# Performance work log

Measured on AMD Instinct MI355X. Metric: run time of the kernel, lower is better.

Reference implementation:

```python
import jax, jax.numpy as jnp
import numpy as np

N_U = 100000; N_I = 100000; D = 64; Q = 5
N_E = 2000000; L = 2; B = 4096; P = 10
TEMP = 0.2; LAM1 = 0.2; LAM2 = 0.2
DROPOUT = 0.1; EPS = 0.1


def setup_inputs() -> dict:
    key = jax.random.key(0)
    ks = jax.random.split(key, 20)
    s = 0.05  # xavier-ish init scale
    return {
        'E_u_0': jax.random.normal(ks[0], (N_U, D), jnp.float32) * s,
        'E_i_0': jax.random.normal(ks[1], (N_I, D), jnp.float32) * s,
        'adj_vals': jax.random.uniform(ks[2], (N_E,), jnp.float32) * 0.05,
        'u_mul_s': jax.random.normal(ks[3], (N_U, Q), jnp.float32) * s,
        'v_mul_s': jax.random.normal(ks[4], (N_I, Q), jnp.float32) * s,
        'ut': jax.random.normal(ks[5], (Q, N_U), jnp.float32) * s,
        'vt': jax.random.normal(ks[6], (Q, N_I), jnp.float32) * s,
        'W_nn': jax.random.normal(ks[7], (D, D), jnp.float32) * s,
        'W_dd': jax.random.normal(ks[8], (D, D), jnp.float32) * s,
        'W_ng': jax.random.normal(ks[9], (L, D, D), jnp.float32) * s,
        'W_dg': jax.random.normal(ks[10], (L, D, D), jnp.float32) * s,
        'W_nd': jax.random.normal(ks[11], (L, D, D), jnp.float32) * s,
        'adj_rows': jax.random.randint(ks[12], (N_E,), 0, N_U),
        'adj_cols': jax.random.randint(ks[13], (N_E,), 0, N_I),
        'uids': jax.random.randint(ks[14], (B,), 0, N_U),
        'iids': jax.random.randint(ks[15], (B,), 0, N_I),
        'pos': jax.random.randint(ks[16], (B, P), 0, N_I),
        'neg': jax.random.randint(ks[17], (B, P), 0, N_I),
    }


def _act(x):  # LeakyReLU(0.5)
    return jnp.where(x >= 0, x, 0.5 * x)


def _l2n(x):  # F.normalize(p=2, dim=1)
    return x / jnp.maximum(jnp.linalg.norm(x, axis=1, keepdims=True), 1e-12)


def _spmm(vals, rows, cols, X, n_out):
    # out[r] = sum_e vals[e] * X[cols[e]]
    return jax.ops.segment_sum(vals[:, None] * X[cols], rows, num_segments=n_out)


def _info_nce(gnn_raw, hyper_raw, W, mask):
    gnn = _l2n(gnn_raw)
    hyper = _l2n(hyper_raw) @ W
    pos_score = jnp.exp(jnp.sum(gnn * hyper, axis=1) / TEMP)
    neg_score = jnp.exp(gnn @ hyper.T / TEMP).sum(axis=1)
    return (-jnp.log(pos_score / (neg_score + 1e-8) + 1e-8) * mask).sum()


def _mk_mask(k):
    return (jax.random.uniform(k, (B,)) > 0.5).astype(jnp.float32)


def _forward(E_u_0, E_i_0, adj_vals, u_mul_s, v_mul_s, ut, vt, W_nn, W_dd, W_ng, W_dg, W_nd,
             adj_rows, adj_cols, uids, iids, pos, neg):
    rkey = jax.random.key(42)
    keep = 1.0 - DROPOUT
    E_u_list = [E_u_0]; E_i_list = [E_i_0]
    Z_u_list = [None]; Z_i_list = [None]
    Z_du_list = [None]; Z_di_list = [None]
    G_u_list = [None]; G_i_list = [None]
    for _ in range(L):
        rkey, k1, k2, k3, k4 = jax.random.split(rkey, 5)
        Eu_p, Ei_p = E_u_list[-1], E_i_list[-1]
        # sparse dropout (independent masks, as in torch code) + spmm + LeakyReLU
        v1 = adj_vals * jax.random.bernoulli(k1, keep, adj_vals.shape) / keep
        Z_du = _act(_spmm(v1, adj_rows, adj_cols, Ei_p, N_U))
        v2 = adj_vals * jax.random.bernoulli(k2, keep, adj_vals.shape) / keep
        Z_di = _act(_spmm(v2, adj_cols, adj_rows, Eu_p, N_I))
        # noise-augmented view
        Z_u = _act(_spmm(adj_vals, adj_rows, adj_cols, Ei_p, N_U))
        Z_u = Z_u + jnp.sign(Z_u) * _l2n(jax.random.uniform(k3, Eu_p.shape)) * EPS
        Z_i = _act(_spmm(adj_vals, adj_cols, adj_rows, Eu_p, N_I))
        Z_i = Z_i + jnp.sign(Z_i) * _l2n(jax.random.uniform(k4, Ei_p.shape)) * EPS
        # SVD (global) view
        G_u = _act(u_mul_s @ (vt @ Ei_p))
        G_i = _act(v_mul_s @ (ut @ Eu_p))
        Z_u_list.append(Z_u); Z_i_list.append(Z_i)
        Z_du_list.append(Z_du); Z_di_list.append(Z_di)
        G_u_list.append(G_u); G_i_list.append(G_i)
        E_u_list.append(Z_u + Z_du + Eu_p)
        E_i_list.append(Z_i + Z_di + Ei_p)
    E_u = E_u_list[0]
    for t in E_u_list[1:]:
        E_u = E_u + t
    E_i = E_i_list[0]
    for t in E_i_list[1:]:
        E_i = E_i + t

    mkey = jax.random.key(7)
    def L_loss(ids, Zl, Gl, Wstack, key):
        out = jnp.float32(0.0)
        for l in range(1, L + 1):
            key, km = jax.random.split(key)
            out = out + _info_nce(Zl[l][ids], Gl[l][ids], Wstack[l - 1], _mk_mask(km))
        return out, key
    def inter_loss(ids, Zl, W, key):
        key, km = jax.random.split(key)
        return _info_nce(Zl[1][ids], Zl[2][ids], W, _mk_mask(km)), key

    loss_n_u, mkey = L_loss(uids, Z_u_list, G_u_list, W_ng, mkey)
    loss_n_i, mkey = L_loss(iids, Z_i_list, G_i_list, W_ng, mkey)
    loss_nn_u, mkey = inter_loss(uids, Z_u_list, W_nn, mkey)
    loss_nn_i, mkey = inter_loss(iids, Z_i_list, W_nn, mkey)
    loss_d_u, mkey = L_loss(uids, Z_du_list, G_u_list, W_dg, mkey)
    loss_d_i, mkey = L_loss(iids, Z_di_list, G_i_list, W_dg, mkey)
    loss_dd_u, mkey = inter_loss(uids, Z_du_list, W_dd, mkey)
    loss_dd_i, mkey = inter_loss(iids, Z_di_list, W_dd, mkey)
    loss_nd_u, mkey = L_loss(uids, Z_u_list, Z_du_list, W_nd, mkey)
    loss_nd_i, mkey = L_loss(iids, Z_i_list, Z_di_list, W_nd, mkey)
    loss_n = loss_n_u + loss_n_i
    loss_d = loss_d_u + loss_d_i
    loss_nn = loss_nn_u + loss_nn_i
    loss_dd = loss_dd_u + loss_dd_i
    loss_nd = loss_nd_u + loss_nd_i

    # U_IConstLoss, vectorized over the batch
    u_emb = E_u[uids]                       # [B, D]
    pos_emb = E_i[pos]                      # [B, P, D]
    neg_emb = E_i[neg]                      # [B, P, D]
    pos_sc = jnp.einsum('bd,bpd->bp', u_emb, pos_emb)
    neg_sc = jnp.einsum('bd,bpd->bp', u_emb, neg_emb)
    pos_d = pos_sc.min(axis=1)
    neg_d = neg_sc.max(axis=1)
    hard = jnp.where(neg_d - pos_d > 0.005, 10.0 * (neg_d - pos_d), 0.0)
    bpr = jnp.maximum(1.0 - pos_sc + neg_sc, 0.0).sum(axis=1)
    loss_r = (bpr + hard).sum() / B

    loss = loss_r + LAM1 * (loss_n + loss_d) + LAM2 * (loss_nn + loss_dd + loss_nd)
    return (loss, loss_r, loss_d, loss_n)


def reference(E_u_0, E_i_0, adj_vals, u_mul_s, v_mul_s, ut, vt, W_nn, W_dd, W_ng, W_dg, W_nd,
              adj_rows, adj_cols, uids, iids, pos, neg):
    return _forward(E_u_0, E_i_0, adj_vals, u_mul_s, v_mul_s, ut, vt, W_nn, W_dd, W_ng, W_dg, W_nd,
                    adj_rows, adj_cols, uids, iids, pos, neg)
```

## Files before the change

kernel.cpp:

```cpp
#include <hip/hip_runtime.h>
#include <hip/hip_bf16.h>
#include <cstdint>

#define C_NU 100000
#define C_NI 100000
#define C_DIM 64
#define C_Q 5
#define C_NE 2000000
#define C_B 4096
#define C_P 10
#define NROW 100000
#define NCB 196
#define NCHK 256
#define CHUNK 7813

typedef unsigned short u16;
typedef unsigned char u8;
typedef __attribute__((ext_vector_type(8))) short short8;
typedef __attribute__((ext_vector_type(4))) float f32x4;

__device__ static inline int rfl(int v) { return __builtin_amdgcn_readfirstlane(v); }
__device__ static inline uint32_t rflu(uint32_t v) {
  return (uint32_t)__builtin_amdgcn_readfirstlane((int)v);
}

__host__ __device__ static inline void tf2x32(uint32_t k0, uint32_t k1,
                                              uint32_t& x0, uint32_t& x1) {
  uint32_t k2 = k0 ^ k1 ^ 0x1BD11BDAu;
#define TFR(r) { x0 += x1; x1 = (x1 << r) | (x1 >> (32 - r)); x1 ^= x0; }
  x0 += k0; x1 += k1;
  TFR(13) TFR(15) TFR(26) TFR(6)
  x0 += k1; x1 += k2 + 1u;
  TFR(17) TFR(29) TFR(16) TFR(24)
  x0 += k2; x1 += k0 + 2u;
  TFR(13) TFR(15) TFR(26) TFR(6)
  x0 += k0; x1 += k1 + 3u;
  TFR(17) TFR(29) TFR(16) TFR(24)
  x0 += k1; x1 += k2 + 4u;
  TFR(13) TFR(15) TFR(26) TFR(6)
  x0 += k2; x1 += k0 + 5u;
#undef TFR
}

__device__ static inline float tf_uniform(uint32_t k0, uint32_t k1, uint32_t idx) {
  uint32_t x0 = 0u, x1 = idx;
  tf2x32(k0, k1, x0, x1);
  uint32_t bits = x0 ^ x1;
  return __uint_as_float((bits >> 9) | 0x3F800000u) - 1.0f;
}

__device__ static inline float leaky(float x) { return x >= 0.f ? x : 0.5f * x; }

__device__ static inline u16 f2bf(float f) {
  uint32_t x = __float_as_uint(f);
  return (u16)((x + 0x7FFFu + ((x >> 16) & 1u)) >> 16);
}
__device__ static inline float bf2f(u16 u) {
  return __uint_as_float((uint32_t)u << 16);
}

__device__ static inline u8 f2fp8(float x) {
  float t = x * 256.f;
  uint32_t sgn = (__float_as_uint(t) >> 24) & 0x80u;
  float a = fabsf(t) * 0x1p-120f;
  uint32_t u = __float_as_uint(a);
  u += 0x7FFFFu + ((u >> 20) & 1u);
  uint32_t mag = u >> 20;
  if (mag > 0x7Fu) mag = 0x7Fu;
  return (u8)(sgn | mag);
}

__constant__ int c_gsel[16] = {0,1,2,3, 0,2, 4,5,6,7, 4,6, 0,1,2,3};
__constant__ int c_hsrc[16] = {8,9,10,11, 1,3, 8,9,10,11, 5,7, 4,5,6,7};
__constant__ int c_wsel[16] = {0,1,0,1, 2,2, 3,4,3,4, 5,5, 6,7,6,7};
__constant__ int c_slot[16] = {0,0,0,0, 2,2, 1,1,1,1, 3,3, 4,4,4,4};

struct WPtrs { const float* W[8]; };
struct NceKeys { uint32_t k0[16]; uint32_t k1[16]; };
struct DropKeys { uint32_t a[8]; };


__global__ __launch_bounds__(256) void passA_hist(
    const int* __restrict__ rows, const int* __restrict__ cols,
    uint32_t* __restrict__ cntA) {
  __shared__ uint32_t h[NCB];
  const int dir = blockIdx.y, c = blockIdx.x, t = threadIdx.x;
  for (int i = t; i < NCB; i += 256) h[i] = 0u;
  __syncthreads();
  const int e0 = c * CHUNK, e1 = min(e0 + CHUNK, C_NE);
  const int* ids = dir ? cols : rows;
  for (int e = e0 + t; e < e1; e += 256) atomicAdd(&h[ids[e] >> 9], 1u);
  __syncthreads();
  for (int i = t; i < NCB; i += 256) cntA[(dir * NCB + i) * NCHK + c] = h[i];
}

__global__ __launch_bounds__(512) void scanA1(
    const uint32_t* __restrict__ cntA, uint32_t* __restrict__ offs,
    uint32_t* __restrict__ bsum) {
  __shared__ uint32_t s[512];
  const int b = blockIdx.x, t = threadIdx.x;
  const int idx = b * 512 + t;
  uint32_t v = cntA[idx];
  s[t] = v;
  __syncthreads();
  for (int off = 1; off < 512; off <<= 1) {
    uint32_t a = (t >= off) ? s[t - off] : 0u;
    __syncthreads();
    s[t] += a;
    __syncthreads();
  }
  offs[idx] = s[t] - v;
  if (t == 511) bsum[b] = s[511];
}

__global__ __launch_bounds__(256) void scanA2(
    const uint32_t* __restrict__ bsum, uint32_t* __restrict__ boff) {
  __shared__ uint32_t s[256];
  const int t = threadIdx.x;
  uint32_t v = (t < NCB) ? bsum[t] : 0u;
  s[t] = v;
  __syncthreads();
  for (int off = 1; off < 256; off <<= 1) {
    uint32_t a = (t >= off) ? s[t - off] : 0u;
    __syncthreads();
    s[t] += a;
    __syncthreads();
  }
  if (t < NCB) boff[t] = s[t] - v;
}

__global__ __launch_bounds__(512) void scanA3(
    uint32_t* __restrict__ offs, const uint32_t* __restrict__ boff) {
  offs[blockIdx.x * 512 + threadIdx.x] += boff[blockIdx.x];
}

__global__ __launch_bounds__(256) void passA_scatter(
    const int* __restrict__ rows, const int* __restrict__ cols,
    const float* __restrict__ vals, const uint32_t* __restrict__ offs,
    uint2* __restrict__ edgesA, DropKeys dk) {
  __shared__ uint32_t lofs[NCB];
  const int dir = blockIdx.y, c = blockIdx.x, t = threadIdx.x;
  for (int i = t; i < NCB; i += 256) lofs[i] = offs[(dir * NCB + i) * NCHK + c];
  __syncthreads();
  const int e0 = c * CHUNK, e1 = min(e0 + CHUNK, C_NE);
  const uint32_t kA0 = dk.a[dir * 4 + 0], kA1 = dk.a[dir * 4 + 1];
  const uint32_t kB0 = dk.a[dir * 4 + 2], kB1 = dk.a[dir * 4 + 3];
  for (int e = e0 + t; e < e1; e += 256) {
    const int r = rows[e], cc = cols[e];
    const int dst = dir ? cc : r, src = dir ? r : cc;
    const uint32_t kl0 = (tf_uniform(kA0, kA1, (uint32_t)e) < 0.9f) ? 1u : 0u;
    const uint32_t kl1 = (tf_uniform(kB0, kB1, (uint32_t)e) < 0.9f) ? 1u : 0u;
    const uint32_t x = (uint32_t)src | (kl0 << 17) | (kl1 << 18) |
                       ((uint32_t)(dst & 511) << 19);
    const uint32_t pos = atomicAdd(&lofs[dst >> 9], 1u);
    edgesA[pos] = make_uint2(x, __float_as_uint(vals[e]));
  }
}

__global__ __launch_bounds__(512) void passB_kernel(
    const uint2* __restrict__ edgesA, const uint32_t* __restrict__ offs,
    uint2* __restrict__ edgesB, uint32_t* __restrict__ starts) {
  __shared__ uint32_t cnt[512];
  __shared__ uint32_t scn[512];
  const int dir = blockIdx.y, cb = blockIdx.x, t = threadIdx.x;
  const uint32_t segStart = offs[(dir * NCB + cb) * NCHK];
  const uint32_t segEnd = (dir == 1 && cb == NCB - 1)
                              ? (uint32_t)(2 * C_NE)
                              : offs[(dir * NCB + cb + 1) * NCHK];
  cnt[t] = 0u;
  __syncthreads();
  for (uint32_t e = segStart + t; e < segEnd; e += 512)
    atomicAdd(&cnt[(edgesA[e].x >> 19) & 511u], 1u);
  __syncthreads();
  uint32_t v = cnt[t];
  scn[t] = v;
  __syncthreads();
  for (int off = 1; off < 512; off <<= 1) {
    uint32_t a = (t >= off) ? scn[t - off] : 0u;
    __syncthreads();
    scn[t] += a;
    __syncthreads();
  }
  const uint32_t rstart = segStart + scn[t] - v;
  const int grow = cb * 512 + t;
  if (grow < NROW) starts[dir * (NROW + 1) + grow] = rstart;
  if (cb == NCB - 1 && t == 0) starts[dir * (NROW + 1) + NROW] = segEnd;
  cnt[t] = rstart;
  __syncthreads();
  for (uint32_t e = segStart + t; e < segEnd; e += 512) {
    const uint2 q = edgesA[e];
    const uint32_t pos = atomicAdd(&cnt[(q.x >> 19) & 511u], 1u);
    edgesB[pos] = q;
  }
}

__global__ __launch_bounds__(256) void fp8_convert(
    const float* __restrict__ src, u8* __restrict__ dst, int n4) {
  int i = blockIdx.x * 256 + threadIdx.x;
  if (i >= n4) return;
  float4 v = ((const float4*)src)[i];
  uint32_t o = (uint32_t)f2fp8(v.x) | ((uint32_t)f2fp8(v.y) << 8) |
               ((uint32_t)f2fp8(v.z) << 16) | ((uint32_t)f2fp8(v.w) << 24);
  ((uint32_t*)dst)[i] = o;
}

__global__ __launch_bounds__(256) void w16_prep(WPtrs wp, u16* __restrict__ Wt16) {
  int i = blockIdx.x * 256 + threadIdx.x;
  if (i >= 8 * 4096) return;
  int w = i >> 12, kd = i & 4095, k = kd >> 6, d = kd & 63;
  Wt16[w * 4096 + d * 64 + k] = f2bf(wp.W[w][k * 64 + d]);
}

__global__ __launch_bounds__(256) void spmm_row(
    const uint2* __restrict__ edges, const uint32_t* __restrict__ starts,
    const u8* __restrict__ Einf, const float* __restrict__ Eprev,
    float* __restrict__ Enext, u8* __restrict__ Enf8,
    u16* __restrict__ Zout, u16* __restrict__ Zdout,
    uint32_t nk0, uint32_t nk1, int layer) {
  const int row = rfl(blockIdx.x * 4 + (threadIdx.x >> 6));
  const int lane = threadIdx.x & 63;
  if (row >= NROW) return;
  const uint32_t s0 = rflu(starts[row]);
  const uint32_t s1 = rflu(starts[row + 1]);
  const uint32_t kbit = 1u << (17 + layer);
  const float VS = 0x1p112f;
  float z = 0.f, zd = 0.f;
  uint32_t e = s0;
  for (; e + 4 <= s1; e += 4) {
    const uint32_t p0 = rflu(edges[e].x),     w0 = rflu(edges[e].y);
    const uint32_t p1 = rflu(edges[e + 1].x), w1 = rflu(edges[e + 1].y);
    const uint32_t p2 = rflu(edges[e + 2].x), w2 = rflu(edges[e + 2].y);
    const uint32_t p3 = rflu(edges[e + 3].x), w3 = rflu(edges[e + 3].y);
    const uint32_t b0 = Einf[(size_t)(p0 & 0x1FFFFu) * 64 + lane];
    const uint32_t b1 = Einf[(size_t)(p1 & 0x1FFFFu) * 64 + lane];
    const uint32_t b2 = Einf[(size_t)(p2 & 0x1FFFFu) * 64 + lane];
    const uint32_t b3 = Einf[(size_t)(p3 & 0x1FFFFu) * 64 + lane];
    const float x0 = __uint_as_float(((b0 & 0x80u) << 24) | ((b0 & 0x7Fu) << 20));
    const float x1 = __uint_as_float(((b1 & 0x80u) << 24) | ((b1 & 0x7Fu) << 20));
    const float x2 = __uint_as_float(((b2 & 0x80u) << 24) | ((b2 & 0x7Fu) << 20));
    const float x3 = __uint_as_float(((b3 & 0x80u) << 24) | ((b3 & 0x7Fu) << 20));
    const float v0 = __uint_as_float(w0) * VS, v1 = __uint_as_float(w1) * VS;
    const float v2 = __uint_as_float(w2) * VS, v3 = __uint_as_float(w3) * VS;
    const float d0 = (p0 & kbit) ? v0 : 0.f;
    const float d1 = (p1 & kbit) ? v1 : 0.f;
    const float d2 = (p2 & kbit) ? v2 : 0.f;
    const float d3 = (p3 & kbit) ? v3 : 0.f;
    z += v0 * x0; zd += d0 * x0;
    z += v1 * x1; zd += d1 * x1;
    z += v2 * x2; zd += d2 * x2;
    z += v3 * x3; zd += d3 * x3;
  }
  for (; e < s1; ++e) {
    const uint32_t p = rflu(edges[e].x), wv = rflu(edges[e].y);
    const uint32_t b = Einf[(size_t)(p & 0x1FFFFu) * 64 + lane];
    const float x = __uint_as_float(((b & 0x80u) << 24) | ((b & 0x7Fu) << 20));
    const float v = __uint_as_float(wv) * VS;
    z += v * x;
    zd += ((p & kbit) ? v : 0.f) * x;
  }
  z = leaky(z);
  zd = leaky(zd * (1.0f / 0.9f));
  const float u = tf_uniform(nk0, nk1, (uint32_t)row * 64u + (uint32_t)lane);
  float ss = u * u;
#pragma unroll
  for (int off = 1; off < 64; off <<= 1) ss += __shfl_xor(ss, off);
  const float nrm = fmaxf(sqrtf(ss), 1e-12f);
  const float sg = (z > 0.f) ? 1.f : (z < 0.f ? -1.f : 0.f);
  z += sg * (u / nrm) * 0.1f;
  const size_t j = (size_t)row * 64 + lane;
  Zout[j] = f2bf(z);
  Zdout[j] = f2bf(zd);
  if (Enext) {
    const float en = z + zd + Eprev[j];
    Enext[j] = en;
    Enf8[j] = f2fp8(en);
  }
}

__global__ __launch_bounds__(256) void svd_reduce2(
    const float* __restrict__ T0, const float* __restrict__ E0,
    const float* __restrict__ T1, const float* __restrict__ E1,
    float* __restrict__ Mu, float* __restrict__ Mi) {
  const int dir = blockIdx.y;
  const float* __restrict__ T = dir ? T1 : T0;
  const float* __restrict__ E = dir ? E1 : E0;
  float* __restrict__ M = dir ? Mi : Mu;
  const int lane = threadIdx.x & 63;
  const int wl = threadIdx.x >> 6;
  const int gw = blockIdx.x * 4 + wl;
  float a0 = 0.f, a1 = 0.f, a2 = 0.f, a3 = 0.f, a4 = 0.f;
  for (int i = gw; i < NROW; i += 4096) {
    const float x = E[(size_t)i * 64 + lane];
    a0 += T[i] * x;
    a1 += T[NROW + i] * x;
    a2 += T[2 * NROW + i] * x;
    a3 += T[3 * NROW + i] * x;
    a4 += T[4 * NROW + i] * x;
  }
  __shared__ float red[4][5][64];
  red[wl][0][lane] = a0; red[wl][1][lane] = a1; red[wl][2][lane] = a2;
  red[wl][3][lane] = a3; red[wl][4][lane] = a4;
  __syncthreads();
  for (int o = threadIdx.x; o < 320; o += 256) {
    const int q = o >> 6, d = o & 63;
    const float s = red[0][q][d] + red[1][q][d] + red[2][q][d] + red[3][q][d];
    atomicAdd(&M[o], s);
  }
}

__global__ __launch_bounds__(256) void gather_norm(
    const int* __restrict__ ids, const u16* __restrict__ Z,
    const u16* __restrict__ Zd, const float* __restrict__ mul_s,
    const float* __restrict__ M, u16* __restrict__ oZ,
    u16* __restrict__ oZd, u16* __restrict__ oG) {
  long long t = (long long)blockIdx.x * blockDim.x + threadIdx.x;
  int b = (int)(t >> 6);
  int d = (int)(t & 63);
  if (b >= C_B) return;
  int id = rfl(ids[b]);
  float v;
  u16* out;
  if (blockIdx.y == 0) { v = bf2f(Z[(size_t)id * 64 + d]); out = oZ; }
  else if (blockIdx.y == 1) { v = bf2f(Zd[(size_t)id * 64 + d]); out = oZd; }
  else {
    float s = 0.f;
#pragma unroll
    for (int q = 0; q < 5; ++q) s += mul_s[(size_t)id * 5 + q] * M[q * 64 + d];
    v = leaky(s);
    out = oG;
  }
  float ss = v * v;
#pragma unroll
  for (int off = 1; off < 64; off <<= 1) ss += __shfl_xor(ss, off);
  float nrm = fmaxf(sqrtf(ss), 1e-12f);
  out[(size_t)b * 64 + d] = f2bf(v / nrm);
}

__global__ __launch_bounds__(256) void hyper_mfma(
    const u16* __restrict__ nb, const u16* __restrict__ Wt16,
    u16* __restrict__ hy) {
  const int call = blockIdx.y;
  const int b0 = blockIdx.x * 64;
  __shared__ u16 Xs[64 * 64];
  __shared__ u16 Ws[64 * 64];
  const int tid = threadIdx.x, lane = tid & 63, wid = tid >> 6;
  const u16* X = nb + (size_t)c_hsrc[call] * C_B * 64;
  const u16* Wt = Wt16 + (size_t)c_wsel[call] * 4096;
  {
    const int r = tid >> 2, seg = tid & 3;
    const int base = r * 128 + seg * 32, sw = (r & 7) << 4;
    const uint4* sx = (const uint4*)&X[(size_t)(b0 + r) * 64 + seg * 16];
    uint4 a = sx[0], b = sx[1];
    *(uint4*)((char*)Xs + (base ^ sw)) = a;
    *(uint4*)((char*)Xs + ((base + 16) ^ sw)) = b;
    const uint4* sv = (const uint4*)&Wt[r * 64 + seg * 16];
    uint4 c = sv[0], d = sv[1];
    *(uint4*)((char*)Ws + (base ^ sw)) = c;
    *(uint4*)((char*)Ws + ((base + 16) ^ sw)) = d;
  }
  __syncthreads();
  const int am = (wid << 4) + (lane & 15);
  short8 af[2];
#pragma unroll
  for (int ks = 0; ks < 2; ++ks) {
    const int off = (am * 128 + ks * 64 + ((lane >> 4) << 4)) ^ ((am & 7) << 4);
    af[ks] = *(const short8*)((const char*)Xs + off);
  }
  const int ob = b0 + (wid << 4) + ((lane >> 4) << 2);
#pragma unroll
  for (int n = 0; n < 4; ++n) {
    const int bn = (n << 4) + (lane & 15);
    f32x4 acc = {0.f, 0.f, 0.f, 0.f};
#pragma unroll
    for (int ks = 0; ks < 2; ++ks) {
      const int off = (bn * 128 + ks * 64 + ((lane >> 4) << 4)) ^ ((bn & 7) << 4);
      short8 bf = *(const short8*)((const char*)Ws + off);
      acc = __builtin_amdgcn_mfma_f32_16x16x32_bf16(af[ks], bf, acc, 0, 0, 0);
    }
    const int d = (n << 4) + (lane & 15);
#pragma unroll
    for (int j = 0; j < 4; ++j)
      hy[(size_t)call * C_B * 64 + (size_t)(ob + j) * 64 + d] =
          f2bf(acc[j] * 7.2134752f);
  }
}

__global__ __launch_bounds__(256) void nce_partial(
    const u16* __restrict__ nb, const u16* __restrict__ hy,
    float* __restrict__ rsbuf, float* __restrict__ psbuf) {
  const int call = blockIdx.z;
  const int jc = blockIdx.y;
  const u16* G = nb + (size_t)c_gsel[call] * C_B * 64;
  const u16* H = hy + (size_t)call * C_B * 64;
  const int br = blockIdx.x * 128;
  const int jt0 = jc * 16;
  __shared__ u16 Gs[128 * 64];
  __shared__ u16 Hs[2][64 * 64];
  const int tid = threadIdx.x, lane = tid & 63, wid = tid >> 6;
  {
    const int r2 = tid >> 1;
    const int sw2 = (r2 & 7) << 4;
#pragma unroll
    for (int p = 0; p < 2; ++p) {
      const int sg = (tid & 1) + p * 2;
      const uint4* src = (const uint4*)&G[(size_t)(br + r2) * 64 + sg * 16];
      uint4 a = src[0], b = src[1];
      const int bse = r2 * 128 + sg * 32;
      *(uint4*)((char*)Gs + (bse ^ sw2)) = a;
      *(uint4*)((char*)Gs + ((bse + 16) ^ sw2)) = b;
    }
  }
  const int r = tid >> 2, seg = tid & 3;
  const int base = r * 128 + seg * 32, sw = (r & 7) << 4;
  {
    const uint4* src = (const uint4*)&H[(size_t)(jt0 * 64 + r) * 64 + seg * 16];
    uint4 a = src[0], b = src[1];
    *(uint4*)((char*)Hs[0] + (base ^ sw)) = a;
    *(uint4*)((char*)Hs[0] + ((base + 16) ^ sw)) = b;
  }
  float rs[2] = {0.f, 0.f}, ps[2] = {0.f, 0.f};
  short8 bfG[2][2];
  const int jt_diag = (blockIdx.x << 1) + (wid >> 1);
  const int hsd0 = (wid & 1) << 1;
  int cur = 0;
  for (int jt = jt0; jt < jt0 + 16; ++jt) {
    __syncthreads();
    if (jt == jt0) {
#pragma unroll
      for (int s = 0; s < 2; ++s)
#pragma unroll
        for (int ks = 0; ks < 2; ++ks) {
          const int gc = (wid << 5) + (s << 4) + (lane & 15);
          const int off = (gc * 128 + ks * 64 + ((lane >> 4) << 4)) ^ ((gc & 7) << 4);
          bfG[s][ks] = *(const short8*)((const char*)Gs + off);
        }
    }
    uint4 na, nb_;
    if (jt + 1 < jt0 + 16) {
      const uint4* src = (const uint4*)&H[(size_t)((jt + 1) * 64 + r) * 64 + seg * 16];
      na = src[0]; nb_ = src[1];
    }
    const bool dj = (jt == jt_diag);
    const char* Hb = (const char*)(Hs[cur]);
#pragma unroll
    for (int hs = 0; hs < 4; ++hs) {
      const int hr = (hs << 4) + (lane & 15);
      const int offA0 = (hr * 128 + ((lane >> 4) << 4)) ^ ((hr & 7) << 4);
      const int offA1 = (hr * 128 + 64 + ((lane >> 4) << 4)) ^ ((hr & 7) << 4);
      const short8 af0 = *(const short8*)(Hb + offA0);
      const short8 af1 = *(const short8*)(Hb + offA1);
      f32x4 acc0 = {0.f, 0.f, 0.f, 0.f}, acc1 = {0.f, 0.f, 0.f, 0.f};
      __builtin_amdgcn_s_setprio(1);
      acc0 = __builtin_amdgcn_mfma_f32_16x16x32_bf16(af0, bfG[0][0], acc0, 0, 0, 0);
      acc0 = __builtin_amdgcn_mfma_f32_16x16x32_bf16(af1, bfG[0][1], acc0, 0, 0, 0);
      acc1 = __builtin_amdgcn_mfma_f32_16x16x32_bf16(af0, bfG[1][0], acc1, 0, 0, 0);
      acc1 = __builtin_amdgcn_mfma_f32_16x16x32_bf16(af1, bfG[1][1], acc1, 0, 0, 0);
      __builtin_amdgcn_s_setprio(0);
      float e0[4], e1[4];
#pragma unroll
      for (int j = 0; j < 4; ++j) {
        e0[j] = exp2f(acc0[j]);
        e1[j] = exp2f(acc1[j]);
      }
      rs[0] += (e0[0] + e0[1]) + (e0[2] + e0[3]);
      rs[1] += (e1[0] + e1[1]) + (e1[2] + e1[3]);
      if (dj) {
        const int jm = (lane & 15) - ((lane >> 4) << 2);
        if (hs == hsd0) {
#pragma unroll
          for (int j = 0; j < 4; ++j)
            if (jm == j) ps[0] = e0[j];
        }
        if (hs == hsd0 + 1) {
#pragma unroll
          for (int j = 0; j < 4; ++j)
            if (jm == j) ps[1] = e1[j];
        }
      }
    }
    if (jt + 1 < jt0 + 16) {
      *(uint4*)((char*)Hs[cur ^ 1] + (base ^ sw)) = na;
      *(uint4*)((char*)Hs[cur ^ 1] + ((base + 16) ^ sw)) = nb_;
    }
    cur ^= 1;
  }
#pragma unroll
  for (int s = 0; s < 2; ++s) {
    rs[s] += __shfl_xor(rs[s], 16); rs[s] += __shfl_xor(rs[s], 32);
    ps[s] += __shfl_xor(ps[s], 16); ps[s] += __shfl_xor(ps[s], 32);
  }
  if ((lane >> 4) == 0) {
    const bool own_diag = ((jt_diag >> 4) == jc);
#pragma unroll
    for (int s = 0; s < 2; ++s) {
      const int gg = br + (wid << 5) + (s << 4) + (lane & 15);
      atomicAdd(&rsbuf[(size_t)call * C_B + gg], rs[s]);
      if (own_diag) psbuf[(size_t)call * C_B + gg] = ps[s];
    }
  }
}

__global__ __launch_bounds__(256) void nce_final(
    const float* __restrict__ rsbuf, const float* __restrict__ psbuf,
    float* __restrict__ slots, NceKeys nk) {
  const int call = blockIdx.y;
  const int g = blockIdx.x * 256 + threadIdx.x;
  const float rs = rsbuf[(size_t)call * C_B + g];
  const float ps = psbuf[(size_t)call * C_B + g];
  const float v = -__logf(ps / (rs + 1e-8f) + 1e-8f);
  const float u = tf_uniform(nk.k0[call], nk.k1[call], (uint32_t)g);
  float c = (u > 0.5f) ? v : 0.f;
#pragma unroll
  for (int off = 1; off < 64; off <<= 1) c += __shfl_xor(c, off);
  __shared__ float wsum[4];
  if ((threadIdx.x & 63) == 0) wsum[threadIdx.x >> 6] = c;
  __syncthreads();
  if (threadIdx.x == 0)
    atomicAdd(&slots[c_slot[call]], wsum[0] + wsum[1] + wsum[2] + wsum[3]);
}

__global__ __launch_bounds__(256) void loss_r_kernel(
    const float* __restrict__ E0u, const float* __restrict__ Eu1,
    const u16* __restrict__ Zu, const u16* __restrict__ Zdu,
    const float* __restrict__ E0i, const float* __restrict__ Ei1,
    const u16* __restrict__ Zi, const u16* __restrict__ Zdi,
    const int* __restrict__ uids, const int* __restrict__ pos,
    const int* __restrict__ neg, float* __restrict__ slots) {
  long long t = (long long)blockIdx.x * blockDim.x + threadIdx.x;
  int b = (int)(t >> 6);
  int d = (int)(t & 63);
  if (b >= C_B) return;
  size_t ju = (size_t)rfl(uids[b]) * 64 + d;
  float u = E0u[ju] + 2.f * Eu1[ju] + bf2f(Zu[ju]) + bf2f(Zdu[ju]);
  float bpr = 0.f, pmin = 3.4e38f, nmax = -3.4e38f;
  for (int p = 0; p < C_P; ++p) {
    size_t jp = (size_t)rfl(pos[b * C_P + p]) * 64 + d;
    size_t jn = (size_t)rfl(neg[b * C_P + p]) * 64 + d;
    float pe = E0i[jp] + 2.f * Ei1[jp] + bf2f(Zi[jp]) + bf2f(Zdi[jp]);
    float ne = E0i[jn] + 2.f * Ei1[jn] + bf2f(Zi[jn]) + bf2f(Zdi[jn]);
    float psc = u * pe, nsc = u * ne;
#pragma unroll
    for (int off = 1; off < 64; off <<= 1) {
      psc += __shfl_xor(psc, off);
      nsc += __shfl_xor(nsc, off);
    }
    pmin = fminf(pmin, psc);
    nmax = fmaxf(nmax, nsc);
    bpr += fmaxf(1.f - psc + nsc, 0.f);
  }
  if (d == 0) {
    float hd = (nmax - pmin > 0.005f) ? 10.f * (nmax - pmin) : 0.f;
    atomicAdd(&slots[5], bpr + hd);
  }
}

__global__ void final_kernel(const float* __restrict__ slots, float* __restrict__ out) {
  if (threadIdx.x == 0 && blockIdx.x == 0) {
    float n = slots[0], dl = slots[1], nn = slots[2], dd = slots[3], nd = slots[4];
    float lr = slots[5] / (float)C_B;
    out[0] = lr + 0.2f * (n + dl) + 0.2f * (nn + dd + nd);
    out[1] = lr;
    out[2] = dl;
    out[3] = n;
  }
}

extern "C" void kernel_launch(void* const* d_in, const int* in_sizes, int n_in,
                              void* d_out, int out_size, void* d_ws, size_t ws_size,
                              hipStream_t stream) {
  (void)in_sizes; (void)n_in; (void)out_size;
  const float* E_u_0   = (const float*)d_in[0];
  const float* E_i_0   = (const float*)d_in[1];
  const float* adjvals = (const float*)d_in[2];
  const float* u_mul_s = (const float*)d_in[3];
  const float* v_mul_s = (const float*)d_in[4];
  const float* ut      = (const float*)d_in[5];
  const float* vt      = (const float*)d_in[6];
  const float* W_nn    = (const float*)d_in[7];
  const float* W_dd    = (const float*)d_in[8];
  const float* W_ng    = (const float*)d_in[9];
  const float* W_dg    = (const float*)d_in[10];
  const float* W_nd    = (const float*)d_in[11];
  const int* adj_rows  = (const int*)d_in[12];
  const int* adj_cols  = (const int*)d_in[13];
  const int* uids      = (const int*)d_in[14];
  const int* iids      = (const int*)d_in[15];
  const int* pos       = (const int*)d_in[16];
  const int* neg       = (const int*)d_in[17];
  float* out = (float*)d_out;

  const size_t NU64 = (size_t)C_NU * 64;
  const size_t NI64 = (size_t)C_NI * 64;
  const size_t B64  = (size_t)C_B * 64;

  float* w = (float*)d_ws;
  float* Eu1 = w; w += NU64;
  float* Ei1 = w; w += NI64;
  u16* Zu  = (u16*)w;
  u16* Zdu = Zu + NU64;
  u16* Zi  = Zdu + NU64;
  u16* Zdi = Zi + NI64;
  w += 2 * NU64;
  float* Mu = w; w += 512;
  float* Mi = w; w += 512;
  u16* normbuf16 = (u16*)w; w += 6 * B64;
  float* slots = w; w += 16;
  uint2* edgesB = (uint2*)w; w += 4 * C_NE;
  u16* hyper16 = (u16*)edgesB;
  u16* Wt16 = (u16*)w; w += 16384;
  uint32_t* cntA = (uint32_t*)w; w += NCB * NCHK * 2;
  uint32_t* offs = (uint32_t*)w; w += NCB * NCHK * 2;
  uint32_t* bsumA = (uint32_t*)w; w += NCB;
  uint32_t* boffA = (uint32_t*)w; w += NCB;
  uint32_t* startsAbs = (uint32_t*)w; w += 2 * (NROW + 1);
  u8* Eu0f = (u8*)w; w += NU64 / 4;
  u8* Ei0f = (u8*)w; w += NI64 / 4;
  u8* Eu1f = (u8*)w; w += NU64 / 4;
  u8* Ei1f = Ei0f;
  float* rsbuf = w; w += 16 * C_B;
  float* psbuf = w; w += 16 * C_B;
  uint2* edgesA = (uint2*)Zu;
  if ((size_t)((char*)w - (char*)d_ws) > ws_size) return;

  auto ksplit = [](uint32_t a, uint32_t b, uint32_t idx, uint32_t& o0, uint32_t& o1) {
    uint32_t x0 = 0u, x1 = idx;
    tf2x32(a, b, x0, x1);
    o0 = x0; o1 = x1;
  };
  uint32_t rk0 = 0u, rk1 = 42u;
  uint32_t lk[2][4][2];
  for (int l = 0; l < 2; ++l) {
    uint32_t n0, n1;
    ksplit(rk0, rk1, 0u, n0, n1);
    for (int i = 0; i < 4; ++i) ksplit(rk0, rk1, (uint32_t)(i + 1), lk[l][i][0], lk[l][i][1]);
    rk0 = n0; rk1 = n1;
  }
  NceKeys nk;
  {
    uint32_t mk0 = 0u, mk1 = 7u;
    for (int i = 0; i < 16; ++i) {
      uint32_t n0, n1;
      ksplit(mk0, mk1, 0u, n0, n1);
      ksplit(mk0, mk1, 1u, nk.k0[i], nk.k1[i]);
      mk0 = n0; mk1 = n1;
    }
  }
  DropKeys dk;
  dk.a[0] = lk[0][0][0]; dk.a[1] = lk[0][0][1];
  dk.a[2] = lk[1][0][0]; dk.a[3] = lk[1][0][1];
  dk.a[4] = lk[0][1][0]; dk.a[5] = lk[0][1][1];
  dk.a[6] = lk[1][1][0]; dk.a[7] = lk[1][1][1];
  WPtrs wp;
  wp.W[0] = W_ng; wp.W[1] = W_ng + 4096;
  wp.W[2] = W_nn;
  wp.W[3] = W_dg; wp.W[4] = W_dg + 4096;
  wp.W[5] = W_dd;
  wp.W[6] = W_nd; wp.W[7] = W_nd + 4096;

  hipMemsetAsync(slots, 0, 16 * 4, stream);
  hipMemsetAsync(rsbuf, 0, 16 * C_B * 4, stream);
  passA_hist<<<dim3(NCHK, 2), 256, 0, stream>>>(adj_rows, adj_cols, cntA);
  scanA1<<<NCB, 512, 0, stream>>>(cntA, offs, bsumA);
  scanA2<<<1, 256, 0, stream>>>(bsumA, boffA);
  scanA3<<<NCB, 512, 0, stream>>>(offs, boffA);
  passA_scatter<<<dim3(NCHK, 2), 256, 0, stream>>>(
      adj_rows, adj_cols, adjvals, offs, edgesA, dk);
  passB_kernel<<<dim3(NCB, 2), 512, 0, stream>>>(edgesA, offs, edgesB, startsAbs);
  fp8_convert<<<(int)(NU64 / 4 + 255) / 256, 256, 0, stream>>>(E_u_0, Eu0f, (int)(NU64 / 4));
  fp8_convert<<<(int)(NI64 / 4 + 255) / 256, 256, 0, stream>>>(E_i_0, Ei0f, (int)(NI64 / 4));
  w16_prep<<<(8 * 4096 + 255) / 256, 256, 0, stream>>>(wp, Wt16);

  const int gb = (int)(B64 / 256);
  const int sb = (NROW + 3) / 4;

  for (int l = 0; l < 2; ++l) {
    hipMemsetAsync(Mu, 0, 1024 * 4, stream);
    svd_reduce2<<<dim3(1024, 2), 256, 0, stream>>>(
        vt, (l == 0) ? E_i_0 : Ei1, ut, (l == 0) ? E_u_0 : Eu1, Mu, Mi);
    spmm_row<<<sb, 256, 0, stream>>>(
        edgesB, startsAbs, (l == 0) ? Ei0f : Ei1f,
        (l == 0) ? E_u_0 : nullptr, (l == 0) ? Eu1 : nullptr,
        (l == 0) ? Eu1f : nullptr, Zu, Zdu, lk[l][2][0], lk[l][2][1], l);
    spmm_row<<<sb, 256, 0, stream>>>(
        edgesB, startsAbs + (NROW + 1), (l == 0) ? Eu0f : Eu1f,
        (l == 0) ? E_i_0 : nullptr, (l == 0) ? Ei1 : nullptr,
        (l == 0) ? Ei1f : nullptr, Zi, Zdi, lk[l][3][0], lk[l][3][1], l);
    gather_norm<<<dim3(gb, 3), 256, 0, stream>>>(
        uids, Zu, Zdu, u_mul_s, Mu,
        normbuf16 + (size_t)(0 + l) * B64, normbuf16 + (size_t)(4 + l) * B64,
        normbuf16 + (size_t)(8 + l) * B64);
    gather_norm<<<dim3(gb, 3), 256, 0, stream>>>(
        iids, Zi, Zdi, v_mul_s, Mi,
        normbuf16 + (size_t)(2 + l) * B64, normbuf16 + (size_t)(6 + l) * B64,
        normbuf16 + (size_t)(10 + l) * B64);
  }

  hyper_mfma<<<dim3(C_B / 64, 16), 256, 0, stream>>>(normbuf16, Wt16, hyper16);
  nce_partial<<<dim3(C_B / 128, 4, 16), 256, 0, stream>>>(normbuf16, hyper16,
                                                          rsbuf, psbuf);
  nce_final<<<dim3(C_B / 256, 16), 256, 0, stream>>>(rsbuf, psbuf, slots, nk);
  loss_r_kernel<<<gb, 256, 0, stream>>>(E_u_0, Eu1, Zu, Zdu, E_i_0, Ei1, Zi, Zdi,
                                        uids, pos, neg, slots);
  final_kernel<<<1, 1, 0, stream>>>(slots, out);
}
```

Measured before the change: 655.2 us.

## Merge user/item SpMM launches, drop LDS staging in MFMA kernels, use raw v_exp

The two per-direction spmm_row launches are merged into one 2D grid that picks its pointers from a struct by blockIdx.y, saving one launch per layer and letting both directions share the GPU. hyper_mfma and nce_partial now load MFMA operands straight from global memory into registers instead of staging them through swizzled shared memory, which removes LDS traffic and a barrier. exp2f is replaced by the raw v_exp_f32 instruction, dropping the range-handling code around it. The risks are uncoalesced global operand loads and slightly different exp behaviour for extreme inputs.

```diff
diff --git a/kernel.cpp b/kernel.cpp
--- a/kernel.cpp
+++ b/kernel.cpp
@@ -22,6 +22,12 @@
 __device__ static inline int rfl(int v) { return __builtin_amdgcn_readfirstlane(v); }
 __device__ static inline uint32_t rflu(uint32_t v) {
   return (uint32_t)__builtin_amdgcn_readfirstlane((int)v);
+}
+
+__device__ static inline float fast_exp2(float x) {
+  float r;
+  asm("v_exp_f32 %0, %1" : "=v"(r) : "v"(x));
+  return r;
 }
 
 __host__ __device__ static inline void tf2x32(uint32_t k0, uint32_t k1,
@@ -78,6 +84,15 @@
 struct WPtrs { const float* W[8]; };
 struct NceKeys { uint32_t k0[16]; uint32_t k1[16]; };
 struct DropKeys { uint32_t a[8]; };
+struct SpmmArgs {
+  const u8* Einf[2];
+  const float* Eprev[2];
+  float* Enext[2];
+  u8* Enf8[2];
+  u16* Z[2];
+  u16* Zd[2];
+  uint32_t nk[2][2];
+};
 
 
 __global__ __launch_bounds__(256) void passA_hist(
@@ -212,14 +227,14 @@
 }
 
 __global__ __launch_bounds__(256) void spmm_row(
-    const uint2* __restrict__ edges, const uint32_t* __restrict__ starts,
-    const u8* __restrict__ Einf, const float* __restrict__ Eprev,
-    float* __restrict__ Enext, u8* __restrict__ Enf8,
-    u16* __restrict__ Zout, u16* __restrict__ Zdout,
-    uint32_t nk0, uint32_t nk1, int layer) {
+    const uint2* __restrict__ edges, const uint32_t* __restrict__ startsAbs,
+    SpmmArgs a, int layer) {
+  const int dir = blockIdx.y;
   const int row = rfl(blockIdx.x * 4 + (threadIdx.x >> 6));
   const int lane = threadIdx.x & 63;
   if (row >= NROW) return;
+  const uint32_t* starts = startsAbs + dir * (NROW + 1);
+  const u8* __restrict__ Einf = a.Einf[dir];
   const uint32_t s0 = rflu(starts[row]);
   const uint32_t s1 = rflu(starts[row + 1]);
   const uint32_t kbit = 1u << (17 + layer);
@@ -260,7 +275,8 @@
   }
   z = leaky(z);
   zd = leaky(zd * (1.0f / 0.9f));
-  const float u = tf_uniform(nk0, nk1, (uint32_t)row * 64u + (uint32_t)lane);
+  const float u = tf_uniform(a.nk[dir][0], a.nk[dir][1],
+                             (uint32_t)row * 64u + (uint32_t)lane);
   float ss = u * u;
 #pragma unroll
   for (int off = 1; off < 64; off <<= 1) ss += __shfl_xor(ss, off);
@@ -268,12 +284,12 @@
   const float sg = (z > 0.f) ? 1.f : (z < 0.f ? -1.f : 0.f);
   z += sg * (u / nrm) * 0.1f;
   const size_t j = (size_t)row * 64 + lane;
-  Zout[j] = f2bf(z);
-  Zdout[j] = f2bf(zd);
-  if (Enext) {
-    const float en = z + zd + Eprev[j];
-    Enext[j] = en;
-    Enf8[j] = f2fp8(en);
+  a.Z[dir][j] = f2bf(z);
+  a.Zd[dir][j] = f2bf(zd);
+  if (a.Enext[dir]) {
+    const float en = z + zd + a.Eprev[dir][j];
+    a.Enext[dir][j] = en;
+    a.Enf8[dir][j] = f2fp8(en);
   }
 }
 
@@ -341,31 +357,15 @@
     u16* __restrict__ hy) {
   const int call = blockIdx.y;
   const int b0 = blockIdx.x * 64;
-  __shared__ u16 Xs[64 * 64];
-  __shared__ u16 Ws[64 * 64];
-  const int tid = threadIdx.x, lane = tid & 63, wid = tid >> 6;
+  const int lane = threadIdx.x & 63, wid = threadIdx.x >> 6;
   const u16* X = nb + (size_t)c_hsrc[call] * C_B * 64;
   const u16* Wt = Wt16 + (size_t)c_wsel[call] * 4096;
-  {
-    const int r = tid >> 2, seg = tid & 3;
-    const int base = r * 128 + seg * 32, sw = (r & 7) << 4;
-    const uint4* sx = (const uint4*)&X[(size_t)(b0 + r) * 64 + seg * 16];
-    uint4 a = sx[0], b = sx[1];
-    *(uint4*)((char*)Xs + (base ^ sw)) = a;
-    *(uint4*)((char*)Xs + ((base + 16) ^ sw)) = b;
-    const uint4* sv = (const uint4*)&Wt[r * 64 + seg * 16];
-    uint4 c = sv[0], d = sv[1];
-    *(uint4*)((char*)Ws + (base ^ sw)) = c;
-    *(uint4*)((char*)Ws + ((base + 16) ^ sw)) = d;
-  }
-  __syncthreads();
   const int am = (wid << 4) + (lane & 15);
+  const int ke = ((lane >> 4) << 3);
   short8 af[2];
 #pragma unroll
-  for (int ks = 0; ks < 2; ++ks) {
-    const int off = (am * 128 + ks * 64 + ((lane >> 4) << 4)) ^ ((am & 7) << 4);
-    af[ks] = *(const short8*)((const char*)Xs + off);
-  }
+  for (int ks = 0; ks < 2; ++ks)
+    af[ks] = *(const short8*)&X[(size_t)(b0 + am) * 64 + ks * 32 + ke];
   const int ob = b0 + (wid << 4) + ((lane >> 4) << 2);
 #pragma unroll
   for (int n = 0; n < 4; ++n) {
@@ -373,8 +373,7 @@
     f32x4 acc = {0.f, 0.f, 0.f, 0.f};
 #pragma unroll
     for (int ks = 0; ks < 2; ++ks) {
-      const int off = (bn * 128 + ks * 64 + ((lane >> 4) << 4)) ^ ((bn & 7) << 4);
-      short8 bf = *(const short8*)((const char*)Ws + off);
+      short8 bf = *(const short8*)&Wt[(size_t)bn * 64 + ks * 32 + ke];
       acc = __builtin_amdgcn_mfma_f32_16x16x32_bf16(af[ks], bf, acc, 0, 0, 0);
     }
     const int d = (n << 4) + (lane & 15);
@@ -394,22 +393,17 @@
   const u16* H = hy + (size_t)call * C_B * 64;
   const int br = blockIdx.x * 128;
   const int jt0 = jc * 16;
-  __shared__ u16 Gs[128 * 64];
   __shared__ u16 Hs[2][64 * 64];
   const int tid = threadIdx.x, lane = tid & 63, wid = tid >> 6;
-  {
-    const int r2 = tid >> 1;
-    const int sw2 = (r2 & 7) << 4;
-#pragma unroll
-    for (int p = 0; p < 2; ++p) {
-      const int sg = (tid & 1) + p * 2;
-      const uint4* src = (const uint4*)&G[(size_t)(br + r2) * 64 + sg * 16];
-      uint4 a = src[0], b = src[1];
-      const int bse = r2 * 128 + sg * 32;
-      *(uint4*)((char*)Gs + (bse ^ sw2)) = a;
-      *(uint4*)((char*)Gs + ((bse + 16) ^ sw2)) = b;
-    }
-  }
+  const int ke = ((lane >> 4) << 3);
+  short8 bfG[2][2];
+#pragma unroll
+  for (int s = 0; s < 2; ++s)
+#pragma unroll
+    for (int ks = 0; ks < 2; ++ks) {
+      const int gc = (wid << 5) + (s << 4) + (lane & 15);
+      bfG[s][ks] = *(const short8*)&G[(size_t)(br + gc) * 64 + ks * 32 + ke];
+    }
   const int r = tid >> 2, seg = tid & 3;
   const int base = r * 128 + seg * 32, sw = (r & 7) << 4;
   {
@@ -419,22 +413,11 @@
     *(uint4*)((char*)Hs[0] + ((base + 16) ^ sw)) = b;
   }
   float rs[2] = {0.f, 0.f}, ps[2] = {0.f, 0.f};
-  short8 bfG[2][2];
   const int jt_diag = (blockIdx.x << 1) + (wid >> 1);
   const int hsd0 = (wid & 1) << 1;
   int cur = 0;
   for (int jt = jt0; jt < jt0 + 16; ++jt) {
     __syncthreads();
-    if (jt == jt0) {
-#pragma unroll
-      for (int s = 0; s < 2; ++s)
-#pragma unroll
-        for (int ks = 0; ks < 2; ++ks) {
-          const int gc = (wid << 5) + (s << 4) + (lane & 15);
-          const int off = (gc * 128 + ks * 64 + ((lane >> 4) << 4)) ^ ((gc & 7) << 4);
-          bfG[s][ks] = *(const short8*)((const char*)Gs + off);
-        }
-    }
     uint4 na, nb_;
     if (jt + 1 < jt0 + 16) {
       const uint4* src = (const uint4*)&H[(size_t)((jt + 1) * 64 + r) * 64 + seg * 16];
@@ -459,8 +442,8 @@
       float e0[4], e1[4];
 #pragma unroll
       for (int j = 0; j < 4; ++j) {
-        e0[j] = exp2f(acc0[j]);
-        e1[j] = exp2f(acc1[j]);
+        e0[j] = fast_exp2(acc0[j]);
+        e1[j] = fast_exp2(acc1[j]);
       }
       rs[0] += (e0[0] + e0[1]) + (e0[2] + e0[3]);
       rs[1] += (e1[0] + e1[1]) + (e1[2] + e1[3]);
@@ -677,14 +660,20 @@
     hipMemsetAsync(Mu, 0, 1024 * 4, stream);
     svd_reduce2<<<dim3(1024, 2), 256, 0, stream>>>(
         vt, (l == 0) ? E_i_0 : Ei1, ut, (l == 0) ? E_u_0 : Eu1, Mu, Mi);
-    spmm_row<<<sb, 256, 0, stream>>>(
-        edgesB, startsAbs, (l == 0) ? Ei0f : Ei1f,
-        (l == 0) ? E_u_0 : nullptr, (l == 0) ? Eu1 : nullptr,
-        (l == 0) ? Eu1f : nullptr, Zu, Zdu, lk[l][2][0], lk[l][2][1], l);
-    spmm_row<<<sb, 256, 0, stream>>>(
-        edgesB, startsAbs + (NROW + 1), (l == 0) ? Eu0f : Eu1f,
-        (l == 0) ? E_i_0 : nullptr, (l == 0) ? Ei1 : nullptr,
-        (l == 0) ? Ei1f : nullptr, Zi, Zdi, lk[l][3][0], lk[l][3][1], l);
+    SpmmArgs sa;
+    sa.Einf[0] = (l == 0) ? Ei0f : Ei1f;
+    sa.Einf[1] = (l == 0) ? Eu0f : Eu1f;
+    sa.Eprev[0] = (l == 0) ? E_u_0 : nullptr;
+    sa.Eprev[1] = (l == 0) ? E_i_0 : nullptr;
+    sa.Enext[0] = (l == 0) ? Eu1 : nullptr;
+    sa.Enext[1] = (l == 0) ? Ei1 : nullptr;
+    sa.Enf8[0] = (l == 0) ? Eu1f : nullptr;
+    sa.Enf8[1] = (l == 0) ? Ei1f : nullptr;
+    sa.Z[0] = Zu; sa.Zd[0] = Zdu;
+    sa.Z[1] = Zi; sa.Zd[1] = Zdi;
+    sa.nk[0][0] = lk[l][2][0]; sa.nk[0][1] = lk[l][2][1];
+    sa.nk[1][0] = lk[l][3][0]; sa.nk[1][1] = lk[l][3][1];
+    spmm_row<<<dim3(sb, 2), 256, 0, stream>>>(edgesB, startsAbs, sa, l);
     gather_norm<<<dim3(gb, 3), 256, 0, stream>>>(
         uids, Zu, Zdu, u_mul_s, Mu,
         normbuf16 + (size_t)(0 + l) * B64, normbuf16 + (size_t)(4 + l) * B64,
```

New measurement: 625.4 us. 4.5% less time.
